# Optimization experiments

Measured on AMD Instinct MI355X. Metric: run time of the kernel, lower is better.

The kernel has to match this reference:

```python
import jax, jax.numpy as jnp
import numpy as np
import math

DIM = 512
NUM_HEADS = 8
DIM_HEAD = DIM // NUM_HEADS


def normalized_coords(h, w):
    # (h*w, 2) with (x, y) in [0, 1]
    y = jnp.linspace(0.0, 1.0, h)
    x = jnp.linspace(0.0, 1.0, w)
    yg, xg = jnp.meshgrid(y, x, indexing='ij')
    return jnp.stack([xg.ravel(), yg.ravel()], axis=-1)


def rotate_half(x):
    dh = x.shape[-1] // 2
    return jnp.concatenate([-x[..., dh:], x[..., :dh]], axis=-1)


def apply_rope(t, coords):
    # t: (n, heads, seq, dim_head); coords: (seq, 2) (identical across batch)
    dim_half = t.shape[-1] // 2
    freq = 1.0 / (10000.0 ** (jnp.arange(dim_half, dtype=jnp.float32) / dim_half))
    ang_x = coords[:, 0:1] * freq  # (seq, dim_half)
    ang_y = coords[:, 1:2] * freq
    ang = jnp.concatenate([ang_x, ang_y], axis=-1)  # (seq, dim_head)
    cos, sin = jnp.cos(ang), jnp.sin(ang)
    return t * cos + rotate_half(t) * sin


def setup_inputs() -> dict:
    key = jax.random.key(0)
    ks = jax.random.split(key, 12)
    n, Np, d, H, W = 4, 1024, DIM, 64, 64
    s = 0.02
    return {
        'local_feat': jax.random.normal(ks[0], (n, Np, d), jnp.float32),
        'global_feat': jax.random.normal(ks[1], (n, d, H, W), jnp.float32),
        'Wq': jax.random.normal(ks[2], (d, d), jnp.float32) * s,
        'bq': jnp.zeros((d,), jnp.float32),
        'Wk': jax.random.normal(ks[3], (d, d), jnp.float32) * s,
        'bk': jnp.zeros((d,), jnp.float32),
        'Wv': jax.random.normal(ks[4], (d, d), jnp.float32) * s,
        'bv': jnp.zeros((d,), jnp.float32),
        'Wg': jax.random.normal(ks[5], (d, 2 * d), jnp.float32) * s,
        'bg': jnp.zeros((d,), jnp.float32),
        'Wo': jax.random.normal(ks[6], (d, d), jnp.float32) * s,
        'bo': jnp.zeros((d,), jnp.float32),
    }


def reference(local_feat, global_feat, Wq, bq, Wk, bk, Wv, bv, Wg, bg, Wo, bo):
    n, Np, d = local_feat.shape
    _, _, H, W = global_feat.shape
    h, dh = NUM_HEADS, DIM_HEAD
    gf = global_feat.reshape(n, d, H * W).transpose(0, 2, 1)  # (n, HW, d)

    P = int(math.isqrt(Np))
    local_coords = normalized_coords(P, P)      # (Np, 2)
    global_coords = normalized_coords(H, W)     # (HW, 2)

    def proj(x, Wt, b):
        return x @ Wt.T + b

    Q = proj(local_feat, Wq, bq).reshape(n, Np, h, dh).transpose(0, 2, 1, 3)
    K = proj(gf, Wk, bk).reshape(n, H * W, h, dh).transpose(0, 2, 1, 3)
    V = proj(gf, Wv, bv).reshape(n, H * W, h, dh).transpose(0, 2, 1, 3)

    Q = apply_rope(Q, local_coords)
    K = apply_rope(K, global_coords)

    scores = jnp.einsum('bhqd,bhkd->bhqk', Q, K) / math.sqrt(dh)
    attn = jax.nn.softmax(scores, axis=-1)
    ao = jnp.einsum('bhqk,bhkd->bhqd', attn, V)
    ao = ao.transpose(0, 2, 1, 3).reshape(n, Np, d)

    gate = jax.nn.sigmoid(jnp.concatenate([local_feat, ao], axis=-1) @ Wg.T + bg)
    enhanced = local_feat + gate * ao
    return enhanced @ Wo.T + bo
```

## Files before the change

kernel.cpp:

```cpp
#include <hip/hip_runtime.h>
#include <hip/hip_bf16.h>
#include <cstdint>

typedef __hip_bfloat16 BF;
typedef unsigned short ushort_t;
typedef __attribute__((ext_vector_type(8))) __bf16 bf16x8;
typedef __attribute__((ext_vector_type(4))) float f32x4;

__device__ __forceinline__ float bu2f(ushort_t u) {
  return __uint_as_float((unsigned)u << 16);
}
__device__ __forceinline__ unsigned pk2(float a, float b) {
  union { __hip_bfloat162 h; unsigned u; } c;
  c.h = __float22bfloat162_rn(make_float2(a, b));
  return c.u;
}
__device__ __forceinline__ unsigned short f2bu(float f) {
  union { BF b; unsigned short u; } c; c.b = __float2bfloat16(f); return c.u;
}
__device__ __forceinline__ float b2f(BF x) { return __bfloat162float(x); }
__device__ __forceinline__ void rd16f(const float* fp, ushort_t* out) {
#pragma unroll
  for (int j = 0; j < 16; j += 4) {
    float4 v = *(const float4*)(fp + j);
    ((unsigned*)out)[j / 2] = pk2(v.x, v.y);
    ((unsigned*)out)[j / 2 + 1] = pk2(v.z, v.w);
  }
}

#define QS 0.1803368801111f

__global__ __launch_bounds__(256) void pre_k(const float* __restrict__ local,
                                             const float* __restrict__ gfeat,
                                             const float* __restrict__ Wq,
                                             const float* __restrict__ bq,
                                             BF* __restrict__ gfT,
                                             BF* __restrict__ Qb) {
  __shared__ __align__(16) ushort_t smem[2][64][72];
  const int t = threadIdx.x;
  if (blockIdx.x < 2048) {
    auto T = smem[0];
    const int g = blockIdx.x;
    const int bz = g & 3, mt = (g >> 2) & 63, kt = g >> 8;
    {
      int krow = t >> 2, mg = t & 3;
      ushort_t vals[16];
      rd16f(gfeat + (size_t)bz * 512 * 4096 + (size_t)(kt * 64 + krow) * 4096 +
                mt * 64 + mg * 16,
            vals);
#pragma unroll
      for (int j = 0; j < 16; ++j) T[mg * 16 + j][krow] = vals[j];
    }
    __syncthreads();
    int mrow = t >> 2, kg = t & 3;
    uint4 a = *(const uint4*)&T[mrow][kg * 16];
    uint4 b = *(const uint4*)&T[mrow][kg * 16 + 8];
    size_t o = ((size_t)bz * 4096 + mt * 64 + mrow) * 512 + kt * 64 + kg * 16;
    *(uint4*)&gfT[o] = a;
    *(uint4*)&gfT[o + 8] = b;
    return;
  }
  auto As = smem[0];
  auto Bs = smem[1];
  const int bx = blockIdx.x - 2048;
  const int m0 = (bx & 63) * 64, n0 = (bx >> 6) * 64;
  const int w = t >> 6, lane = t & 63;
  const int quad = lane >> 4, l16 = lane & 15;

  f32x4 acc[4] = {};
  for (int k0 = 0; k0 < 512; k0 += 64) {
    __syncthreads();
    {
      int row = t >> 2, cg = t & 3;
      int kg = k0 + cg * 16;
      ushort_t vals[16];
      rd16f(local + (size_t)(m0 + row) * 512 + kg, vals);
      *(uint4*)&As[row][cg * 16] = *(uint4*)&vals[0];
      *(uint4*)&As[row][cg * 16 + 8] = *(uint4*)&vals[8];
      ushort_t bv[16];
      rd16f(Wq + (size_t)(n0 + row) * 512 + kg, bv);
      *(uint4*)&Bs[row][cg * 16] = *(uint4*)&bv[0];
      *(uint4*)&Bs[row][cg * 16 + 8] = *(uint4*)&bv[8];
    }
    __syncthreads();
#pragma unroll
    for (int kc = 0; kc < 2; ++kc) {
      bf16x8 af = *(const bf16x8*)&As[w * 16 + l16][kc * 32 + quad * 8];
#pragma unroll
      for (int nt = 0; nt < 4; ++nt) {
        bf16x8 bfv = *(const bf16x8*)&Bs[nt * 16 + l16][kc * 32 + quad * 8];
        acc[nt] = __builtin_amdgcn_mfma_f32_16x16x32_bf16(af, bfv, acc[nt], 0, 0, 0);
      }
    }
  }
  const int head = n0 >> 6;
#pragma unroll
  for (int r = 0; r < 4; ++r) {
    int mg = m0 + w * 16 + quad * 4 + r;
    int bb = mg >> 10, qi = mg & 1023;
    float x = (float)(qi & 31) * (1.f / 31.f);
    float y = (float)(qi >> 5) * (1.f / 31.f);
    size_t base = (((size_t)bb * 8 + head) * 1024 + qi) * 64;
#pragma unroll
    for (int j = 0; j < 2; ++j) {
      int c0 = j * 16 + l16;
      float t0 = acc[j][r] + bq[head * 64 + c0];
      float t1 = acc[j + 2][r] + bq[head * 64 + c0 + 32];
      float fr = __expf((float)c0 * (-9.210340371976184f / 32.f));
      float ax = x * fr, ay = y * fr;
      Qb[base + c0] = __float2bfloat16((t0 * __cosf(ax) - t1 * __sinf(ax)) * QS);
      Qb[base + c0 + 32] = __float2bfloat16((t1 * __cosf(ay) + t0 * __sinf(ay)) * QS);
    }
  }
}

__global__ __launch_bounds__(256) void kv_k(const BF* __restrict__ gfT,
                                            const float* __restrict__ Wk,
                                            const float* __restrict__ Wv,
                                            const float* __restrict__ bk,
                                            const float* __restrict__ bv,
                                            BF* __restrict__ Kb,
                                            BF* __restrict__ VTb) {
  __shared__ __align__(16) ushort_t smem[2][128][72];
  auto As = smem[0];
  auto Bs = smem[1];
  const int tid = threadIdx.x;
  const int w = tid >> 6, lane = tid & 63;
  const int quad = lane >> 4, l16 = lane & 15;
  const int wm = w >> 1, wn = w & 1;
  const int g = blockIdx.x;
  const int a = g & 7, y = (g >> 3) & 7, bidx = g >> 6;
  const int m0 = ((bidx << 1) | (a & 1)) * 128;
  const int n0 = y * 128;
  const int bz = a >> 1;

  f32x4 acc[4][4] = {};
  for (int k0 = 0; k0 < 512; k0 += 64) {
    __syncthreads();
#pragma unroll
    for (int u = 0; u < 2; ++u) {
      int unit = tid + u * 256;
      int row = unit >> 2, cg = unit & 3;
      const uint4* p = (const uint4*)(gfT + ((size_t)bz * 4096 + m0 + row) * 512 +
                                      k0 + cg * 16);
      *(uint4*)&As[row][cg * 16] = p[0];
      *(uint4*)&As[row][cg * 16 + 8] = p[1];
    }
#pragma unroll
    for (int u = 0; u < 2; ++u) {
      int unit = tid + u * 256;
      int row = unit >> 2, cg = unit & 3;
      const float* bsrc = (n0 >= 512) ? Wv : Wk;
      size_t nrow = (n0 >= 512) ? (n0 - 512 + row) : (n0 + row);
      ushort_t vals[16];
      rd16f(bsrc + nrow * 512 + k0 + cg * 16, vals);
      *(uint4*)&Bs[row][cg * 16] = *(uint4*)&vals[0];
      *(uint4*)&Bs[row][cg * 16 + 8] = *(uint4*)&vals[8];
    }
    __syncthreads();
#pragma unroll
    for (int kc = 0; kc < 2; ++kc) {
      bf16x8 af[4], bfv[4];
#pragma unroll
      for (int i = 0; i < 4; ++i) {
        af[i] = *(const bf16x8*)&As[wm * 64 + i * 16 + l16][kc * 32 + quad * 8];
        bfv[i] = *(const bf16x8*)&Bs[wn * 64 + i * 16 + l16][kc * 32 + quad * 8];
      }
#pragma unroll
      for (int mt = 0; mt < 4; ++mt)
#pragma unroll
        for (int nt = 0; nt < 4; ++nt)
          acc[mt][nt] = __builtin_amdgcn_mfma_f32_16x16x32_bf16(af[mt], bfv[nt], acc[mt][nt], 0, 0, 0);
    }
  }
  if (n0 < 512) {
    const int head = (n0 + wn * 64) >> 6;
#pragma unroll
    for (int mt = 0; mt < 4; ++mt)
#pragma unroll
      for (int r = 0; r < 4; ++r) {
        int pg = m0 + wm * 64 + mt * 16 + quad * 4 + r;
        float x = (float)(pg & 63) * (1.f / 63.f);
        float yy = (float)(pg >> 6) * (1.f / 63.f);
        size_t base = (((size_t)bz * 8 + head) * 4096 + pg) * 64;
#pragma unroll
        for (int j = 0; j < 2; ++j) {
          int c0 = j * 16 + l16;
          float t0 = acc[mt][j][r] + bk[head * 64 + c0];
          float t1 = acc[mt][j + 2][r] + bk[head * 64 + c0 + 32];
          float fr = __expf((float)c0 * (-9.210340371976184f / 32.f));
          float ax = x * fr, ay = yy * fr;
          Kb[base + c0] = __float2bfloat16(t0 * __cosf(ax) - t1 * __sinf(ax));
          Kb[base + c0 + 32] = __float2bfloat16(t1 * __cosf(ay) + t0 * __sinf(ay));
        }
      }
  } else {
    const int n0v = n0 - 512;
    __syncthreads();
    ushort_t (*T)[136] = (ushort_t(*)[136]) & smem[0][0][0];
#pragma unroll
    for (int mt = 0; mt < 4; ++mt)
#pragma unroll
      for (int nt = 0; nt < 4; ++nt)
#pragma unroll
        for (int r = 0; r < 4; ++r) {
          int n_l = wn * 64 + nt * 16 + l16;
          int m_l = wm * 64 + mt * 16 + quad * 4 + r;
          T[n_l][m_l] = f2bu(acc[mt][nt][r] + bv[n0v + n_l]);
        }
    __syncthreads();
    int row = tid >> 1, half = tid & 1;
    size_t gbase = (((size_t)bz * 8 + (n0v >> 6) + (row >> 6)) * 64 + (row & 63)) * 4096 +
                   m0 + half * 64;
    uint4* dst = (uint4*)(VTb + gbase);
    const uint4* src = (const uint4*)&T[row][half * 64];
#pragma unroll
    for (int j = 0; j < 8; ++j) dst[j] = src[j];
  }
}

template <int NS>
__global__ __launch_bounds__(256) void attn_k(const BF* __restrict__ Q,
                                              const BF* __restrict__ K,
                                              const BF* __restrict__ VT,
                                              BF* __restrict__ AO,
                                              BF* __restrict__ Opart,
                                              float* __restrict__ lpart) {
  __shared__ __align__(16) ushort_t Ks[64][64];
  __shared__ __align__(16) ushort_t VTs[64][64];
  __shared__ __align__(16) ushort_t Ps[4][32][64];

  const int tid = threadIdx.x;
  const int w = tid >> 6, lane = tid & 63;
  const int quad = lane >> 4, l16 = lane & 15;
  const int r3 = l16 & 7;
  const int sc0 = (quad ^ r3) << 3;
  const int sc1 = sc0 ^ 32;

  const int g = blockIdx.x;
  const int bh = g & 31;
  const int qt = (g >> 5) & 7;
  const int ks = g >> 8;
  const int b = bh >> 3, h = bh & 7;
  const int q0 = qt * 128 + w * 32;
  const int kspan = 4096 / NS, kbase = ks * kspan;

  bf16x8 qa[2][2];
#pragma unroll
  for (int qs = 0; qs < 2; ++qs) {
    const BF* qp = Q + (((size_t)bh << 10) + q0 + qs * 16 + l16) * 64 + quad * 8;
    qa[qs][0] = *(const bf16x8*)qp;
    qa[qs][1] = *(const bf16x8*)(qp + 32);
  }
  bf16x8 ones;
#pragma unroll
  for (int j = 0; j < 8; ++j) ones[j] = (__bf16)1.0f;

  const BF* Kp = K + (size_t)bh * 4096 * 64;
  const BF* VTp = VT + (size_t)bh * 64 * 4096;

  f32x4 o[2][4] = {};
  f32x4 ol[2] = {};

  const int srow = tid >> 2, scol = (tid & 3) * 16;
  const int ssc = ((2 * (tid & 3)) ^ (srow & 7)) << 3;
  {
    const uint4* kp = (const uint4*)(Kp + (size_t)(kbase + srow) * 64 + scol);
    const uint4* vp = (const uint4*)(VTp + (size_t)srow * 4096 + kbase + scol);
    uint4 a = kp[0], bb = kp[1], c = vp[0], d = vp[1];
    *(uint4*)&Ks[srow][ssc] = a;  *(uint4*)&Ks[srow][ssc ^ 8] = bb;
    *(uint4*)&VTs[srow][ssc] = c; *(uint4*)&VTs[srow][ssc ^ 8] = d;
  }

  for (int c0k = kbase; c0k < kbase + kspan; c0k += 64) {
    __syncthreads();
    uint4 nk0, nk1, nv0, nv1;
    const bool more = (c0k + 64 < kbase + kspan);
    if (more) {
      const uint4* kp = (const uint4*)(Kp + (size_t)(c0k + 64 + srow) * 64 + scol);
      const uint4* vp = (const uint4*)(VTp + (size_t)srow * 4096 + c0k + 64 + scol);
      nk0 = kp[0]; nk1 = kp[1]; nv0 = vp[0]; nv1 = vp[1];
    }

#pragma unroll
    for (int ct = 0; ct < 4; ++ct) {
      const int krow = ct * 16 + l16;
      bf16x8 kb0 = *(const bf16x8*)&Ks[krow][sc0];
      bf16x8 kb1 = *(const bf16x8*)&Ks[krow][sc1];
#pragma unroll
      for (int qs = 0; qs < 2; ++qs) {
        f32x4 s = {};
        __builtin_amdgcn_s_setprio(1);
        s = __builtin_amdgcn_mfma_f32_16x16x32_bf16(kb0, qa[qs][0], s, 0, 0, 0);
        s = __builtin_amdgcn_mfma_f32_16x16x32_bf16(kb1, qa[qs][1], s, 0, 0, 0);
        __builtin_amdgcn_s_setprio(0);
        uint2 uu;
        uu.x = pk2(__builtin_exp2f(s[0]), __builtin_exp2f(s[1]));
        uu.y = pk2(__builtin_exp2f(s[2]), __builtin_exp2f(s[3]));
        *(uint2*)&Ps[w][qs * 16 + l16][(ct * 16 + quad * 4) ^ (r3 << 3)] = uu;
      }
    }

#pragma unroll
    for (int qs = 0; qs < 2; ++qs) {
      const ushort_t* pr = &Ps[w][qs * 16 + l16][0];
      bf16x8 pa0 = *(const bf16x8*)(pr + sc0);
      bf16x8 pa1 = *(const bf16x8*)(pr + sc1);
      __builtin_amdgcn_s_setprio(1);
      ol[qs] = __builtin_amdgcn_mfma_f32_16x16x32_bf16(ones, pa0, ol[qs], 0, 0, 0);
      ol[qs] = __builtin_amdgcn_mfma_f32_16x16x32_bf16(ones, pa1, ol[qs], 0, 0, 0);
#pragma unroll
      for (int nt = 0; nt < 4; ++nt) {
        const int vrow = nt * 16 + l16;
        bf16x8 vb0 = *(const bf16x8*)&VTs[vrow][sc0];
        bf16x8 vb1 = *(const bf16x8*)&VTs[vrow][sc1];
        o[qs][nt] = __builtin_amdgcn_mfma_f32_16x16x32_bf16(vb0, pa0, o[qs][nt], 0, 0, 0);
        o[qs][nt] = __builtin_amdgcn_mfma_f32_16x16x32_bf16(vb1, pa1, o[qs][nt], 0, 0, 0);
      }
      __builtin_amdgcn_s_setprio(0);
    }

    __syncthreads();
    if (more) {
      *(uint4*)&Ks[srow][ssc] = nk0;  *(uint4*)&Ks[srow][ssc ^ 8] = nk1;
      *(uint4*)&VTs[srow][ssc] = nv0; *(uint4*)&VTs[srow][ssc ^ 8] = nv1;
    }
  }

#pragma unroll
  for (int qs = 0; qs < 2; ++qs) {
    int qg = q0 + qs * 16 + l16;
    if (NS == 1) {
      float invl = 1.f / ol[qs][0];
#pragma unroll
      for (int nt = 0; nt < 4; ++nt) {
        uint2 uu;
        uu.x = pk2(o[qs][nt][0] * invl, o[qs][nt][1] * invl);
        uu.y = pk2(o[qs][nt][2] * invl, o[qs][nt][3] * invl);
        *(uint2*)(AO + (((size_t)b << 10) + qg) * 512 + h * 64 + nt * 16 + quad * 4) = uu;
      }
    } else {
      if (quad == 0) lpart[ks * 32768 + (bh << 10) + qg] = ol[qs][0];
#pragma unroll
      for (int nt = 0; nt < 4; ++nt) {
        uint2 uu;
        uu.x = pk2(o[qs][nt][0], o[qs][nt][1]);
        uu.y = pk2(o[qs][nt][2], o[qs][nt][3]);
        *(uint2*)(Opart + (size_t)ks * 2097152 + (((size_t)bh << 10) + qg) * 64 +
                  nt * 16 + quad * 4) = uu;
      }
    }
  }
}

template <int NS>
__global__ __launch_bounds__(256) void gate_k(const float* __restrict__ local,
                                              const BF* __restrict__ AO,
                                              const BF* __restrict__ Opart,
                                              const float* __restrict__ lpart,
                                              const float* __restrict__ Wg,
                                              const float* __restrict__ bg,
                                              BF* __restrict__ ENH) {
  __shared__ __align__(16) ushort_t As[64][72];
  __shared__ __align__(16) ushort_t Bs[64][72];
  const int tid = threadIdx.x;
  const int w = tid >> 6, lane = tid & 63;
  const int quad = lane >> 4, l16 = lane & 15;
  const int m0 = blockIdx.x * 64, n0 = blockIdx.y * 64;

  f32x4 acc[4] = {};
  float aosv[4][4];
  for (int k0 = 0; k0 < 1024; k0 += 64) {
    __syncthreads();
    {
      int row = tid >> 2, cg = tid & 3;
      int kg = k0 + cg * 16;
      ushort_t vals[16];
      if (kg < 512) {
        rd16f(local + (size_t)(m0 + row) * 512 + kg, vals);
      } else {
        int c = kg - 512;
        int hh = c >> 6, dh0 = c & 63;
        int mg = m0 + row;
        size_t bq = (size_t)(((mg >> 10) * 8 + hh) << 10) + (mg & 1023);
        if (NS == 1) {
          const uint4* p = (const uint4*)(AO + (size_t)mg * 512 + c);
          *(uint4*)&vals[0] = p[0]; *(uint4*)&vals[8] = p[1];
        } else {
          float ls = 0.f;
#pragma unroll
          for (int s2 = 0; s2 < NS; ++s2) ls += lpart[s2 * 32768 + bq];
          float inv = 1.f / ls;
          float av[16] = {};
#pragma unroll
          for (int s2 = 0; s2 < NS; ++s2) {
            const ushort_t* op = (const ushort_t*)Opart + (size_t)s2 * 2097152 +
                                 bq * 64 + dh0;
            uint4 u0 = ((const uint4*)op)[0], u1 = ((const uint4*)op)[1];
            const ushort_t* pu = (const ushort_t*)&u0;
#pragma unroll
            for (int j = 0; j < 8; ++j) av[j] += bu2f(pu[j]);
            pu = (const ushort_t*)&u1;
#pragma unroll
            for (int j = 0; j < 8; ++j) av[8 + j] += bu2f(pu[j]);
          }
#pragma unroll
          for (int j = 0; j < 16; j += 2)
            ((unsigned*)vals)[j / 2] = pk2(av[j] * inv, av[j + 1] * inv);
        }
      }
      *(uint4*)&As[row][cg * 16] = *(uint4*)&vals[0];
      *(uint4*)&As[row][cg * 16 + 8] = *(uint4*)&vals[8];
      ushort_t bv[16];
      rd16f(Wg + (size_t)(n0 + row) * 1024 + kg, bv);
      *(uint4*)&Bs[row][cg * 16] = *(uint4*)&bv[0];
      *(uint4*)&Bs[row][cg * 16 + 8] = *(uint4*)&bv[8];
    }
    __syncthreads();
    if (k0 == 512 + n0) {
#pragma unroll
      for (int r = 0; r < 4; ++r)
#pragma unroll
        for (int nt = 0; nt < 4; ++nt)
          aosv[r][nt] = bu2f(As[w * 16 + quad * 4 + r][nt * 16 + l16]);
    }
#pragma unroll
    for (int kc = 0; kc < 2; ++kc) {
      bf16x8 af = *(const bf16x8*)&As[w * 16 + l16][kc * 32 + quad * 8];
#pragma unroll
      for (int nt = 0; nt < 4; ++nt) {
        bf16x8 bfv = *(const bf16x8*)&Bs[nt * 16 + l16][kc * 32 + quad * 8];
        acc[nt] = __builtin_amdgcn_mfma_f32_16x16x32_bf16(af, bfv, acc[nt], 0, 0, 0);
      }
    }
  }
#pragma unroll
  for (int r = 0; r < 4; ++r) {
    int mg = m0 + w * 16 + quad * 4 + r;
#pragma unroll
    for (int nt = 0; nt < 4; ++nt) {
      int ng = n0 + nt * 16 + l16;
      size_t idx = (size_t)mg * 512 + ng;
      float gg = 1.f / (1.f + __expf(-(acc[nt][r] + bg[ng])));
      ENH[idx] = __float2bfloat16(local[idx] + gg * aosv[r][nt]);
    }
  }
}

__global__ __launch_bounds__(256) void out_k(const BF* __restrict__ ENH,
                                             const float* __restrict__ Wo,
                                             const float* __restrict__ bo,
                                             float* __restrict__ out) {
  __shared__ __align__(16) ushort_t As[64][72];
  __shared__ __align__(16) ushort_t Bs[64][72];
  const int tid = threadIdx.x;
  const int w = tid >> 6, lane = tid & 63;
  const int quad = lane >> 4, l16 = lane & 15;
  const int m0 = blockIdx.x * 64, n0 = blockIdx.y * 64;

  f32x4 acc[4] = {};
  for (int k0 = 0; k0 < 512; k0 += 64) {
    __syncthreads();
    {
      int row = tid >> 2, cg = tid & 3;
      int kg = k0 + cg * 16;
      const uint4* p = (const uint4*)(ENH + (size_t)(m0 + row) * 512 + kg);
      *(uint4*)&As[row][cg * 16] = p[0];
      *(uint4*)&As[row][cg * 16 + 8] = p[1];
      ushort_t bv[16];
      rd16f(Wo + (size_t)(n0 + row) * 512 + kg, bv);
      *(uint4*)&Bs[row][cg * 16] = *(uint4*)&bv[0];
      *(uint4*)&Bs[row][cg * 16 + 8] = *(uint4*)&bv[8];
    }
    __syncthreads();
#pragma unroll
    for (int kc = 0; kc < 2; ++kc) {
      bf16x8 af = *(const bf16x8*)&As[w * 16 + l16][kc * 32 + quad * 8];
#pragma unroll
      for (int nt = 0; nt < 4; ++nt) {
        bf16x8 bfv = *(const bf16x8*)&Bs[nt * 16 + l16][kc * 32 + quad * 8];
        acc[nt] = __builtin_amdgcn_mfma_f32_16x16x32_bf16(af, bfv, acc[nt], 0, 0, 0);
      }
    }
  }
#pragma unroll
  for (int r = 0; r < 4; ++r) {
    int mg = m0 + w * 16 + quad * 4 + r;
#pragma unroll
    for (int nt = 0; nt < 4; ++nt) {
      int ng = n0 + nt * 16 + l16;
      out[(size_t)mg * 512 + ng] = acc[nt][r] + bo[ng];
    }
  }
}

extern "C" void kernel_launch(void* const* d_in, const int* in_sizes, int n_in,
                              void* d_out, int out_size, void* d_ws, size_t ws_size,
                              hipStream_t stream) {
  const float* local = (const float*)d_in[0];
  const float* gfeat = (const float*)d_in[1];
  const float* Wq = (const float*)d_in[2];
  const float* bq = (const float*)d_in[3];
  const float* Wk = (const float*)d_in[4];
  const float* bk = (const float*)d_in[5];
  const float* Wv = (const float*)d_in[6];
  const float* bv = (const float*)d_in[7];
  const float* Wg = (const float*)d_in[8];
  const float* bg = (const float*)d_in[9];
  const float* Wo = (const float*)d_in[10];
  const float* bo = (const float*)d_in[11];

  char* w = (char*)d_ws;
  BF* Qb = (BF*)w;            w += (size_t)2097152 * 2;
  BF* Kb = (BF*)w;            w += (size_t)8388608 * 2;
  BF* VTb = (BF*)w;           w += (size_t)8388608 * 2;
  BF* AO = (BF*)w;            w += (size_t)2097152 * 2;
  BF* gfT = (BF*)w;
  BF* Opart = (BF*)w;
  size_t baseOff = (size_t)(w - (char*)d_ws);
  BF* ENH = Qb;

  int NS = 1;
  if (baseOff + 4 * (4194304 + 131072) <= ws_size) NS = 4;
  else if (baseOff + 16777216 + 2 * 131072 <= ws_size) NS = 2;
  float* lpart = (float*)(w + (size_t)NS * 4194304);

  dim3 blk(256);
  pre_k<<<dim3(2560), blk, 0, stream>>>(local, gfeat, Wq, bq, gfT, Qb);
  kv_k<<<dim3(1024), blk, 0, stream>>>(gfT, Wk, Wv, bk, bv, Kb, VTb);
  if (NS == 4) {
    attn_k<4><<<dim3(1024), blk, 0, stream>>>(Qb, Kb, VTb, AO, Opart, lpart);
    gate_k<4><<<dim3(64, 8), blk, 0, stream>>>(local, AO, Opart, lpart, Wg, bg, ENH);
  } else if (NS == 2) {
    attn_k<2><<<dim3(512), blk, 0, stream>>>(Qb, Kb, VTb, AO, Opart, lpart);
    gate_k<2><<<dim3(64, 8), blk, 0, stream>>>(local, AO, Opart, lpart, Wg, bg, ENH);
  } else {
    attn_k<1><<<dim3(256), blk, 0, stream>>>(Qb, Kb, VTb, AO, nullptr, nullptr);
    gate_k<1><<<dim3(64, 8), blk, 0, stream>>>(local, AO, Opart, lpart, Wg, bg, ENH);
  }
  out_k<<<dim3(64, 8), blk, 0, stream>>>(ENH, Wo, bo, (float*)d_out);
}
```

Before: 265.6 us.

## Keep softmax probabilities in registers via lane swaps and double-buffer K/V tiles

```diff
diff --git a/kernel.cpp b/kernel.cpp
--- a/kernel.cpp
+++ b/kernel.cpp
@@ -6,6 +6,8 @@
 typedef unsigned short ushort_t;
 typedef __attribute__((ext_vector_type(8))) __bf16 bf16x8;
 typedef __attribute__((ext_vector_type(4))) float f32x4;
+typedef __attribute__((ext_vector_type(2))) unsigned uv2;
+typedef __attribute__((ext_vector_type(4))) unsigned uint4v;
 
 __device__ __forceinline__ float bu2f(ushort_t u) {
   return __uint_as_float((unsigned)u << 16);
@@ -26,6 +28,24 @@
     ((unsigned*)out)[j / 2] = pk2(v.x, v.y);
     ((unsigned*)out)[j / 2 + 1] = pk2(v.z, v.w);
   }
+}
+
+__device__ __forceinline__ void qswapB5(unsigned& a, unsigned& b) {
+  uv2 r = __builtin_amdgcn_permlane32_swap(a, b, false, false);
+  a = r[0]; b = r[1];
+}
+__device__ __forceinline__ void qswapB4(unsigned& a, unsigned& b, int lane) {
+#if __has_builtin(__builtin_amdgcn_permlane16_swap)
+  uv2 r = __builtin_amdgcn_permlane16_swap(a, b, false, false);
+  a = r[0]; b = r[1];
+#else
+  unsigned as = __builtin_amdgcn_ds_swizzle(a, 0x401F);
+  unsigned bs = __builtin_amdgcn_ds_swizzle(b, 0x401F);
+  bool hi = (lane & 16) != 0;
+  unsigned na = hi ? bs : a;
+  unsigned nb = hi ? b : as;
+  a = na; b = nb;
+#endif
 }
 
 #define QS 0.1803368801111f
@@ -220,15 +240,14 @@
 }
 
 template <int NS>
-__global__ __launch_bounds__(256) void attn_k(const BF* __restrict__ Q,
-                                              const BF* __restrict__ K,
-                                              const BF* __restrict__ VT,
-                                              BF* __restrict__ AO,
-                                              BF* __restrict__ Opart,
-                                              float* __restrict__ lpart) {
-  __shared__ __align__(16) ushort_t Ks[64][64];
-  __shared__ __align__(16) ushort_t VTs[64][64];
-  __shared__ __align__(16) ushort_t Ps[4][32][64];
+__global__ __launch_bounds__(256, 4) void attn_k(const BF* __restrict__ Q,
+                                                 const BF* __restrict__ K,
+                                                 const BF* __restrict__ VT,
+                                                 BF* __restrict__ AO,
+                                                 BF* __restrict__ Opart,
+                                                 float* __restrict__ lpart) {
+  __shared__ __align__(16) ushort_t Ks[2][64][64];
+  __shared__ __align__(16) ushort_t VTs[2][64][64];
 
   const int tid = threadIdx.x;
   const int w = tid >> 6, lane = tid & 63;
@@ -268,63 +287,77 @@
     const uint4* kp = (const uint4*)(Kp + (size_t)(kbase + srow) * 64 + scol);
     const uint4* vp = (const uint4*)(VTp + (size_t)srow * 4096 + kbase + scol);
     uint4 a = kp[0], bb = kp[1], c = vp[0], d = vp[1];
-    *(uint4*)&Ks[srow][ssc] = a;  *(uint4*)&Ks[srow][ssc ^ 8] = bb;
-    *(uint4*)&VTs[srow][ssc] = c; *(uint4*)&VTs[srow][ssc ^ 8] = d;
-  }
-
-  for (int c0k = kbase; c0k < kbase + kspan; c0k += 64) {
-    __syncthreads();
+    *(uint4*)&Ks[0][srow][ssc] = a;  *(uint4*)&Ks[0][srow][ssc ^ 8] = bb;
+    *(uint4*)&VTs[0][srow][ssc] = c; *(uint4*)&VTs[0][srow][ssc ^ 8] = d;
+  }
+  __syncthreads();
+
+  const int nc = kspan / 64;
+  for (int c = 0; c < nc; ++c) {
+    const int cur = c & 1;
     uint4 nk0, nk1, nv0, nv1;
-    const bool more = (c0k + 64 < kbase + kspan);
+    const bool more = (c + 1 < nc);
     if (more) {
-      const uint4* kp = (const uint4*)(Kp + (size_t)(c0k + 64 + srow) * 64 + scol);
-      const uint4* vp = (const uint4*)(VTp + (size_t)srow * 4096 + c0k + 64 + scol);
+      const int c1 = kbase + (c + 1) * 64;
+      const uint4* kp = (const uint4*)(Kp + (size_t)(c1 + srow) * 64 + scol);
+      const uint4* vp = (const uint4*)(VTp + (size_t)srow * 4096 + c1 + scol);
       nk0 = kp[0]; nk1 = kp[1]; nv0 = vp[0]; nv1 = vp[1];
     }
 
 #pragma unroll
-    for (int ct = 0; ct < 4; ++ct) {
-      const int krow = ct * 16 + l16;
-      bf16x8 kb0 = *(const bf16x8*)&Ks[krow][sc0];
-      bf16x8 kb1 = *(const bf16x8*)&Ks[krow][sc1];
-#pragma unroll
-      for (int qs = 0; qs < 2; ++qs) {
+    for (int qs = 0; qs < 2; ++qs) {
+      unsigned Sp[4][2];
+#pragma unroll
+      for (int ct = 0; ct < 4; ++ct) {
+        const int krow = ct * 16 + l16;
+        bf16x8 kb0 = *(const bf16x8*)&Ks[cur][krow][sc0];
+        bf16x8 kb1 = *(const bf16x8*)&Ks[cur][krow][sc1];
         f32x4 s = {};
         __builtin_amdgcn_s_setprio(1);
         s = __builtin_amdgcn_mfma_f32_16x16x32_bf16(kb0, qa[qs][0], s, 0, 0, 0);
         s = __builtin_amdgcn_mfma_f32_16x16x32_bf16(kb1, qa[qs][1], s, 0, 0, 0);
         __builtin_amdgcn_s_setprio(0);
-        uint2 uu;
-        uu.x = pk2(__builtin_exp2f(s[0]), __builtin_exp2f(s[1]));
-        uu.y = pk2(__builtin_exp2f(s[2]), __builtin_exp2f(s[3]));
-        *(uint2*)&Ps[w][qs * 16 + l16][(ct * 16 + quad * 4) ^ (r3 << 3)] = uu;
-      }
-    }
-
-#pragma unroll
-    for (int qs = 0; qs < 2; ++qs) {
-      const ushort_t* pr = &Ps[w][qs * 16 + l16][0];
-      bf16x8 pa0 = *(const bf16x8*)(pr + sc0);
-      bf16x8 pa1 = *(const bf16x8*)(pr + sc1);
+        Sp[ct][0] = pk2(__builtin_exp2f(s[0]), __builtin_exp2f(s[1]));
+        Sp[ct][1] = pk2(__builtin_exp2f(s[2]), __builtin_exp2f(s[3]));
+      }
+      unsigned pr[8];
+#pragma unroll
+      for (int hf = 0; hf < 2; ++hf) {
+#pragma unroll
+        for (int hh = 0; hh < 2; ++hh) {
+          unsigned aa = Sp[hf * 2][hh], bb2 = Sp[hf * 2 + 1][hh];
+          qswapB5(aa, bb2);
+          qswapB4(aa, bb2, lane);
+          pr[hf * 4 + hh] = aa;
+          pr[hf * 4 + 2 + hh] = bb2;
+        }
+      }
+      uint4v u0 = {pr[0], pr[1], pr[2], pr[3]};
+      uint4v u1 = {pr[4], pr[5], pr[6], pr[7]};
+      bf16x8 pa0 = __builtin_bit_cast(bf16x8, u0);
+      bf16x8 pa1 = __builtin_bit_cast(bf16x8, u1);
+
       __builtin_amdgcn_s_setprio(1);
       ol[qs] = __builtin_amdgcn_mfma_f32_16x16x32_bf16(ones, pa0, ol[qs], 0, 0, 0);
       ol[qs] = __builtin_amdgcn_mfma_f32_16x16x32_bf16(ones, pa1, ol[qs], 0, 0, 0);
 #pragma unroll
       for (int nt = 0; nt < 4; ++nt) {
         const int vrow = nt * 16 + l16;
-        bf16x8 vb0 = *(const bf16x8*)&VTs[vrow][sc0];
-        bf16x8 vb1 = *(const bf16x8*)&VTs[vrow][sc1];
+        bf16x8 vb0 = *(const bf16x8*)&VTs[cur][vrow][sc0];
+        bf16x8 vb1 = *(const bf16x8*)&VTs[cur][vrow][sc1];
         o[qs][nt] = __builtin_amdgcn_mfma_f32_16x16x32_bf16(vb0, pa0, o[qs][nt], 0, 0, 0);
         o[qs][nt] = __builtin_amdgcn_mfma_f32_16x16x32_bf16(vb1, pa1, o[qs][nt], 0, 0, 0);
       }
       __builtin_amdgcn_s_setprio(0);
     }
 
-    __syncthreads();
     if (more) {
-      *(uint4*)&Ks[srow][ssc] = nk0;  *(uint4*)&Ks[srow][ssc ^ 8] = nk1;
-      *(uint4*)&VTs[srow][ssc] = nv0; *(uint4*)&VTs[srow][ssc ^ 8] = nv1;
-    }
+      *(uint4*)&Ks[cur ^ 1][srow][ssc] = nk0;
+      *(uint4*)&Ks[cur ^ 1][srow][ssc ^ 8] = nk1;
+      *(uint4*)&VTs[cur ^ 1][srow][ssc] = nv0;
+      *(uint4*)&VTs[cur ^ 1][srow][ssc ^ 8] = nv1;
+    }
+    __syncthreads();
   }
 
 #pragma unroll
```

Result: faster. 249.5 us (-6.0%).
